# Kernel tuning notes

Hardware: AMD Instinct MI355X
Metric: run time of the kernel (lower is better)

## Reference

```python
import jax, jax.numpy as jnp
import numpy as np

N, C, H, W, HD = 32, 24, 12, 12, 128
GT, FP, A = 256, 256, 28
DIN = (C + 2) * 2 + HD  # 180, g_theta input dim


def setup_inputs() -> dict:
    key = jax.random.key(0)
    ks = jax.random.split(key, 18)
    def w(k, shape):
        fan_in = shape[0]
        return jax.random.normal(k, shape, jnp.float32) / np.sqrt(fan_in).astype(np.float32)
    inp = {
        "x": jax.random.normal(ks[0], (N, C, H, W), jnp.float32),
        "q": jax.random.normal(ks[1], (N, HD), jnp.float32),
        "gW0": w(ks[2], (DIN, GT)), "gb0": jnp.zeros((GT,), jnp.float32),
        "gW1": w(ks[3], (GT, GT)),  "gb1": jnp.zeros((GT,), jnp.float32),
        "gW2": w(ks[4], (GT, GT)),  "gb2": jnp.zeros((GT,), jnp.float32),
        "gW3": w(ks[5], (GT, GT)),  "gb3": jnp.zeros((GT,), jnp.float32),
        "fW0": w(ks[6], (GT, FP)),  "fb0": jnp.zeros((FP,), jnp.float32),
        "fW1": w(ks[7], (FP, FP)),  "fb1": jnp.zeros((FP,), jnp.float32),
        "fW2": w(ks[8], (FP, A)),   "fb2": jnp.zeros((A,), jnp.float32),
    }
    return inp


def _rn_forward(x, q, gW0, gb0, gW1, gb1, gW2, gb2, gW3, gb3,
                fW0, fb0, fW1, fb1, fW2, fb2):
    n, c, h, w = x.shape
    o = h * w
    # rn_encode: per-object features + (x, y) coordinates in [-1, 1]
    feats = x.reshape(n, c, o).transpose(0, 2, 1)            # [n, o, c]
    xc = jnp.repeat(jnp.linspace(-1.0, 1.0, h), w)           # row coord per pixel
    yc = jnp.tile(jnp.linspace(-1.0, 1.0, w), h)             # col coord per pixel
    coords = jnp.stack([xc, yc], axis=-1).astype(x.dtype)    # [o, 2]
    feats = jnp.concatenate([feats, jnp.broadcast_to(coords, (n, o, 2))], axis=-1)  # [n, o, c+2]
    cp = c + 2
    # pairs[n, a, b] = [feats[b], feats[a], q]  (matches torch unsqueeze(1)/unsqueeze(2))
    pairs = jnp.concatenate([
        jnp.broadcast_to(feats[:, None, :, :], (n, o, o, cp)),
        jnp.broadcast_to(feats[:, :, None, :], (n, o, o, cp)),
        jnp.broadcast_to(q[:, None, None, :], (n, o, o, q.shape[1])),
    ], axis=-1)                                              # [n, o, o, 2*cp+hd]
    # g_theta: 4-layer ReLU MLP applied per pair
    hdd = pairs
    for Wm, b in ((gW0, gb0), (gW1, gb1), (gW2, gb2), (gW3, gb3)):
        hdd = jax.nn.relu(jnp.einsum('nabd,de->nabe', hdd, Wm) + b)
    # lower_sum: keep lower-triangular (incl. diagonal) pairs, sum over them
    mask = jnp.tril(jnp.ones((o, o), hdd.dtype))[None, :, :, None]
    rel = jnp.sum(hdd * mask, axis=(1, 2))                   # [n, GT]
    # f_phi: ReLU hidden layers, linear output (dropout = eval mode no-op)
    y = jax.nn.relu(rel @ fW0 + fb0)
    y = jax.nn.relu(y @ fW1 + fb1)
    logits = y @ fW2 + fb2                                   # [n, A]
    return logits


def reference(x, q, gW0, gb0, gW1, gb1, gW2, gb2, gW3, gb3,
              fW0, fb0, fW1, fb1, fW2, fb2):
    return _rn_forward(x, q, gW0, gb0, gW1, gb1, gW2, gb2, gW3, gb3,
                       fW0, fb0, fW1, fb1, fW2, fb2)
```

## Files before the change

kernel.cpp:

```cpp
#include <hip/hip_runtime.h>
#include <hip/hip_bf16.h>

typedef __attribute__((ext_vector_type(8))) short short8;
typedef __attribute__((ext_vector_type(4))) float f32x4;

#define O 144
#define NB 32
#define GT 256
#define NPAIRS 10440
#define TP 128
#define NT 82
#define GRID (NB*NT)
#define CHUNK 328

#define WS_WT   0u
#define WS_U    393216u
#define WS_V    2752512u
#define WS_REL  5144576u
#define WS_CNT  5177344u

__device__ __forceinline__ unsigned short f2bf(float f){
  unsigned int uu = __builtin_bit_cast(unsigned int, f);
  unsigned int lsb = (uu >> 16) & 1u;
  uu += 0x7fffu + lsb;
  return (unsigned short)(uu >> 16);
}
__device__ __forceinline__ unsigned int cvtpk(float lo, float hi){
  unsigned int r;
  asm("v_cvt_pk_bf16_f32 %0, %1, %2" : "=v"(r) : "v"(lo), "v"(hi));
  return r;
}

__global__ void prep_all(const float* __restrict__ x, const float* __restrict__ q,
                         const float* __restrict__ gW0, const float* __restrict__ gb0,
                         const float* __restrict__ gW1, const float* __restrict__ gW2,
                         const float* __restrict__ gW3,
                         unsigned short* __restrict__ u, unsigned short* __restrict__ v,
                         unsigned short* __restrict__ WtP, float* __restrict__ rel,
                         int* __restrict__ cnt){
  int blk = blockIdx.x, t = threadIdx.x;
  if (blk < 256){
    __shared__ float xs[24][18];
    __shared__ float qs[128];
    int n = blk >> 3, oq = blk & 7;
    int o0 = oq * 18;
    for (int i = t; i < 432; i += 256){
      int c = i / 18, oo = i - c*18;
      xs[c][oo] = x[(n*24 + c)*144 + o0 + oo];
    }
    if (t < 128) qs[t] = q[n*128 + t];
    __syncthreads();
    float wq = gb0[t];
    for (int d = 0; d < 128; d++) wq += qs[d] * gW0[(52 + d)*GT + t];
    float wc[52];
    #pragma unroll
    for (int c = 0; c < 52; c++) wc[c] = gW0[c*GT + t];
    for (int oo = 0; oo < 18; oo++){
      int o = o0 + oo;
      float xc = -1.f + 2.f * (float)(o / 12) / 11.f;
      float yc = -1.f + 2.f * (float)(o % 12) / 11.f;
      float su = wq + xc*wc[24] + yc*wc[25];
      float sv =      xc*wc[50] + yc*wc[51];
      #pragma unroll
      for (int c = 0; c < 24; c++){ float f = xs[c][oo]; su += f*wc[c]; sv += f*wc[26+c]; }
      u[(size_t)(n*O + o)*GT + t] = f2bf(su);
      v[(size_t)(n*O + o)*GT + t] = f2bf(sv);
    }
  } else {
    int b2 = blk - 256;
    int li = b2 >> 8, e = b2 & 255;
    int k = t;
    const float* W = (li == 0) ? gW1 : (li == 1) ? gW2 : gW3;
    int et = e >> 4, r = e & 15;
    int kk = k >> 5, g = (k >> 3) & 3, d = k & 7;
    WtP[li*65536 + et*4096 + kk*512 + r*32 + g*8 + d] = f2bf(W[k*GT + e]);
    if (b2 < NB) rel[b2*GT + t] = 0.f;
    if (b2 == 0 && t < NB) cnt[t] = 0;
  }
}

__global__ __launch_bounds__(256, 2) void rn_main(
    const unsigned short* __restrict__ u, const unsigned short* __restrict__ v,
    const unsigned short* __restrict__ WtP,
    const float* __restrict__ gb1, const float* __restrict__ gb2,
    const float* __restrict__ gb3, float* __restrict__ rel, int* __restrict__ cnt,
    const float* __restrict__ fW0, const float* __restrict__ fb0,
    const float* __restrict__ fW1, const float* __restrict__ fb1,
    const float* __restrict__ fW2, const float* __restrict__ fb2,
    float* __restrict__ out)
{
  __shared__ short8 hbuf[4096];
  char* lds = (char*)hbuf;

  const int tid  = threadIdx.x;
  const int lane = tid & 63;
  const int wav  = tid >> 6;
  int lg = (blockIdx.x & 7)*CHUNK + (blockIdx.x >> 3);
  const int n    = lg / NT;
  const int tile = lg - n*NT;
  const int tbase = tile * TP;
  const int l15 = lane & 15, l4 = lane >> 4;

  const unsigned short* wb = WtP + wav*16384 + l15*32 + l4*8;
  short8 aP0,aP1,aP2,aP3, aQ0,aQ1,aQ2,aQ3;
#define LA(s0,s1,s2,s3,p_) { const unsigned short* _wp = wb + ((p_) >> 3)*65536 + ((p_) & 7)*512; \
    s0 = *(const short8*)(_wp);        s1 = *(const short8*)(_wp + 4096); \
    s2 = *(const short8*)(_wp + 8192); s3 = *(const short8*)(_wp + 12288); }
  LA(aP0,aP1,aP2,aP3, 0)
  LA(aQ0,aQ1,aQ2,aQ3, 1)

  {
    int row = wav*32 + (lane >> 1);
    int pt  = tbase + row;
    bool valid = pt < NPAIRS;
    int pa = 0, pb = 0;
    if (valid){
      pa = (int)((sqrtf(8.f*(float)pt + 1.f) - 1.f) * 0.5f);
      while ((pa + 1)*(pa + 2)/2 <= pt) pa++;
      while (pa*(pa + 1)/2 > pt) pa--;
      pb = pt - pa*(pa + 1)/2;
    }
    const uint4* up4 = (const uint4*)(u + (size_t)(n*O + pb)*GT);
    const uint4* vp4 = (const uint4*)(v + (size_t)(n*O + pa)*GT);
    int half = lane & 1;
    int sbase = row*512 + half*256;
    int ts = ((lane >> 1) & 7) << 4;
    #pragma unroll
    for (int cc = 0; cc < 16; cc++){
      uint4 hv;
      if (valid){
        uint4 uu = up4[half*16 + cc];
        uint4 vv = vp4[half*16 + cc];
        #pragma unroll
        for (int j = 0; j < 4; j++){
          unsigned int ud = (&uu.x)[j], vd = (&vv.x)[j];
          float lo = __builtin_bit_cast(float, ud << 16) + __builtin_bit_cast(float, vd << 16);
          float hi = __builtin_bit_cast(float, ud & 0xffff0000u) + __builtin_bit_cast(float, vd & 0xffff0000u);
          (&hv.x)[j] = cvtpk(fmaxf(lo, 0.f), fmaxf(hi, 0.f));
        }
      } else {
        hv = (uint4){0u, 0u, 0u, 0u};
      }
      *(uint4*)(lds + sbase + ((cc*16) ^ ts)) = hv;
    }
  }
  __syncthreads();

  const bool fullvalid = (tbase + TP <= NPAIRS);
  const int swz01 = (l15 & 3) << 4;
  const int swz2  = (l15 & 4) << 4;
  const int rbE = l15*512 + ((l4*16) ^ swz01) + swz2;
  const int rbO = l15*512 + ((l4*16) ^ swz01) - swz2;
  const int ebase = l15*512 + wav*128 + ((l4*8) ^ ((l15 & 1) << 4)) + ((l15 & 6) << 4);
  f32x4 acc[4][8];
  short8 b0[8], b1[8];

#define LOADB(dst_, kk_) { const int rb_ = ((kk_) & 1) ? rbO : rbE; \
    _Pragma("unroll") \
    for (int jp = 0; jp < 8; jp++) dst_[jp] = *(short8*)(lds + rb_ + jp*8192 + (kk_)*64); }

#define MFMAB(bb_, s0,s1,s2,s3) { \
    __builtin_amdgcn_s_setprio(1); \
    _Pragma("unroll") \
    for (int jp = 0; jp < 8; jp++){ \
      acc[0][jp] = __builtin_amdgcn_mfma_f32_16x16x32_bf16(s0, bb_[jp], acc[0][jp], 0, 0, 0); \
      acc[1][jp] = __builtin_amdgcn_mfma_f32_16x16x32_bf16(s1, bb_[jp], acc[1][jp], 0, 0, 0); \
      acc[2][jp] = __builtin_amdgcn_mfma_f32_16x16x32_bf16(s2, bb_[jp], acc[2][jp], 0, 0, 0); \
      acc[3][jp] = __builtin_amdgcn_mfma_f32_16x16x32_bf16(s3, bb_[jp], acc[3][jp], 0, 0, 0); } \
    __builtin_amdgcn_s_setprio(0); }

  #pragma unroll
  for (int L = 0; L < 3; L++){
    const float* gb = (L == 0) ? gb1 : (L == 1) ? gb2 : gb3;

    #pragma unroll
    for (int ie = 0; ie < 4; ie++){
      f32x4 bbv = *(const f32x4*)(gb + wav*64 + ie*16 + l4*4);
      #pragma unroll
      for (int jp = 0; jp < 8; jp++) acc[ie][jp] = bbv;
    }

    LOADB(b0, 0);
    #pragma unroll
    for (int kk = 0; kk < 8; kk++){
      const int p  = L*8 + kk;
      const int pn = (p + 2 > 23) ? 23 : p + 2;
      short8 c0,c1,c2,c3;
      if (p & 1){ c0=aQ0; c1=aQ1; c2=aQ2; c3=aQ3; }
      else      { c0=aP0; c1=aP1; c2=aP2; c3=aP3; }
      if (kk < 7){ if (kk & 1) { LOADB(b0, kk + 1) } else { LOADB(b1, kk + 1) } }
      if (p & 1){ LA(aQ0,aQ1,aQ2,aQ3, pn) } else { LA(aP0,aP1,aP2,aP3, pn) }
      if (kk & 1){ MFMAB(b1, c0,c1,c2,c3) } else { MFMAB(b0, c0,c1,c2,c3) }
    }

    if (L < 2){
      __syncthreads();
      #pragma unroll
      for (int ie = 0; ie < 4; ie++){
        int ea = ebase ^ (ie*32);
        #pragma unroll
        for (int jp = 0; jp < 8; jp++){
          uint2 pk;
          pk.x = cvtpk(fmaxf(acc[ie][jp][0], 0.f), fmaxf(acc[ie][jp][1], 0.f));
          pk.y = cvtpk(fmaxf(acc[ie][jp][2], 0.f), fmaxf(acc[ie][jp][3], 0.f));
          *(uint2*)(lds + ea + jp*8192) = pk;
        }
      }
      __syncthreads();
    } else {
      #pragma unroll
      for (int ie = 0; ie < 4; ie++){
        int e0 = wav*64 + ie*16 + l4*4;
        f32x4 s = {0.f, 0.f, 0.f, 0.f};
        #pragma unroll
        for (int jp = 0; jp < 8; jp++){
          bool pv = fullvalid || (tbase + jp*16 + l15 < NPAIRS);
          #pragma unroll
          for (int j = 0; j < 4; j++){
            float hvv = fmaxf(acc[ie][jp][j], 0.f);
            s[j] += pv ? hvv : 0.f;
          }
        }
        #pragma unroll
        for (int st = 1; st < 16; st <<= 1){
          #pragma unroll
          for (int j = 0; j < 4; j++)
            s[j] += __shfl_xor(s[j], st);
        }
        if (l15 == 0){
          #pragma unroll
          for (int j = 0; j < 4; j++)
            atomicAdd(&rel[n*GT + e0 + j], s[j]);
        }
      }
    }
  }
#undef LA
#undef LOADB
#undef MFMAB

  __syncthreads();
  if (tid == 0) ((int*)lds)[0] = atomicAdd(&cnt[n], 1);
  __syncthreads();
  int done = ((int*)lds)[0];
  __syncthreads();
  if (done == NT - 1){
    float rv = atomicAdd(&rel[n*GT + tid], 0.f);
    float* hsm = (float*)lds;
    float* ysm = hsm + 256;
    int t = tid;
    hsm[t] = rv;
    __syncthreads();
    float s = fb0[t];
    for (int k = 0; k < 256; k++) s += hsm[k] * fW0[k*GT + t];
    ysm[t] = fmaxf(s, 0.f);
    __syncthreads();
    s = fb1[t];
    for (int k = 0; k < 256; k++) s += ysm[k] * fW1[k*GT + t];
    __syncthreads();
    hsm[t] = fmaxf(s, 0.f);
    __syncthreads();
    if (t < 28){
      s = fb2[t];
      for (int k = 0; k < 256; k++) s += hsm[k] * fW2[k*28 + t];
      out[n*28 + t] = s;
    }
  }
}

extern "C" void kernel_launch(void* const* d_in, const int* in_sizes, int n_in,
                              void* d_out, int out_size, void* d_ws, size_t ws_size,
                              hipStream_t stream){
  (void)in_sizes; (void)n_in; (void)out_size; (void)ws_size;
  const float* x   = (const float*)d_in[0];
  const float* q   = (const float*)d_in[1];
  const float* gW0 = (const float*)d_in[2];
  const float* gb0 = (const float*)d_in[3];
  const float* gW1 = (const float*)d_in[4];
  const float* gb1 = (const float*)d_in[5];
  const float* gW2 = (const float*)d_in[6];
  const float* gb2 = (const float*)d_in[7];
  const float* gW3 = (const float*)d_in[8];
  const float* gb3 = (const float*)d_in[9];
  const float* fW0 = (const float*)d_in[10];
  const float* fb0 = (const float*)d_in[11];
  const float* fW1 = (const float*)d_in[12];
  const float* fb1 = (const float*)d_in[13];
  const float* fW2 = (const float*)d_in[14];
  const float* fb2 = (const float*)d_in[15];

  char* ws = (char*)d_ws;
  unsigned short* WtP = (unsigned short*)(ws + WS_WT);
  unsigned short* u   = (unsigned short*)(ws + WS_U);
  unsigned short* v   = (unsigned short*)(ws + WS_V);
  float* rel = (float*)(ws + WS_REL);
  int*   cnt = (int*)(ws + WS_CNT);
  float* out = (float*)d_out;

  hipLaunchKernelGGL(prep_all, dim3(1024), dim3(256), 0, stream,
                     x, q, gW0, gb0, gW1, gW2, gW3, u, v, WtP, rel, cnt);
  hipLaunchKernelGGL(rn_main, dim3(GRID), dim3(256), 0, stream,
                     u, v, WtP, gb1, gb2, gb3, rel, cnt,
                     fW0, fb0, fW1, fb1, fW2, fb2, out);
}
```

Baseline: 260.5 us.

## Split B-fragment loads into halves and shrink A prefetch to one stage

The main MFMA loop now loads the LDS B operand in two halves of four fragments, interleaving each half-load with the MFMAs on the other half, and prefetches the weight A fragments only one K-step ahead instead of two. This lowers register pressure (fewer live short8 buffers) to ease spilling or scheduling at two waves per SIMD, at the cost of less latency hiding for global weight loads. Separately, the prep kernel now computes u/v with one block per batch (32 blocks) instead of 256 blocks, which loads the whole image into LDS but leaves much less parallelism for that phase.

```diff
diff --git a/kernel.cpp b/kernel.cpp
--- a/kernel.cpp
+++ b/kernel.cpp
@@ -39,15 +39,11 @@
                          unsigned short* __restrict__ WtP, float* __restrict__ rel,
                          int* __restrict__ cnt){
   int blk = blockIdx.x, t = threadIdx.x;
-  if (blk < 256){
-    __shared__ float xs[24][18];
+  if (blk < NB){
+    __shared__ float xs[24*144];
     __shared__ float qs[128];
-    int n = blk >> 3, oq = blk & 7;
-    int o0 = oq * 18;
-    for (int i = t; i < 432; i += 256){
-      int c = i / 18, oo = i - c*18;
-      xs[c][oo] = x[(n*24 + c)*144 + o0 + oo];
-    }
+    int n = blk;
+    for (int i = t; i < 24*144; i += 256) xs[i] = x[n*24*144 + i];
     if (t < 128) qs[t] = q[n*128 + t];
     __syncthreads();
     float wq = gb0[t];
@@ -55,19 +51,18 @@
     float wc[52];
     #pragma unroll
     for (int c = 0; c < 52; c++) wc[c] = gW0[c*GT + t];
-    for (int oo = 0; oo < 18; oo++){
-      int o = o0 + oo;
+    for (int o = 0; o < O; o++){
       float xc = -1.f + 2.f * (float)(o / 12) / 11.f;
       float yc = -1.f + 2.f * (float)(o % 12) / 11.f;
       float su = wq + xc*wc[24] + yc*wc[25];
       float sv =      xc*wc[50] + yc*wc[51];
       #pragma unroll
-      for (int c = 0; c < 24; c++){ float f = xs[c][oo]; su += f*wc[c]; sv += f*wc[26+c]; }
+      for (int c = 0; c < 24; c++){ float f = xs[c*144 + o]; su += f*wc[c]; sv += f*wc[26+c]; }
       u[(size_t)(n*O + o)*GT + t] = f2bf(su);
       v[(size_t)(n*O + o)*GT + t] = f2bf(sv);
     }
   } else {
-    int b2 = blk - 256;
+    int b2 = blk - NB;
     int li = b2 >> 8, e = b2 & 255;
     int k = t;
     const float* W = (li == 0) ? gW1 : (li == 1) ? gW2 : gW3;
@@ -102,12 +97,11 @@
   const int l15 = lane & 15, l4 = lane >> 4;
 
   const unsigned short* wb = WtP + wav*16384 + l15*32 + l4*8;
-  short8 aP0,aP1,aP2,aP3, aQ0,aQ1,aQ2,aQ3;
-#define LA(s0,s1,s2,s3,p_) { const unsigned short* _wp = wb + ((p_) >> 3)*65536 + ((p_) & 7)*512; \
-    s0 = *(const short8*)(_wp);        s1 = *(const short8*)(_wp + 4096); \
-    s2 = *(const short8*)(_wp + 8192); s3 = *(const short8*)(_wp + 12288); }
-  LA(aP0,aP1,aP2,aP3, 0)
-  LA(aQ0,aQ1,aQ2,aQ3, 1)
+  short8 an0, an1, an2, an3;
+#define LOADA(p_) { const unsigned short* _wp = wb + ((p_) >> 3)*65536 + ((p_) & 7)*512; \
+    an0 = *(const short8*)(_wp);        an1 = *(const short8*)(_wp + 4096); \
+    an2 = *(const short8*)(_wp + 8192); an3 = *(const short8*)(_wp + 12288); }
+  LOADA(0);
 
   {
     int row = wav*32 + (lane >> 1);
@@ -153,20 +147,20 @@
   const int rbO = l15*512 + ((l4*16) ^ swz01) - swz2;
   const int ebase = l15*512 + wav*128 + ((l4*8) ^ ((l15 & 1) << 4)) + ((l15 & 6) << 4);
   f32x4 acc[4][8];
-  short8 b0[8], b1[8];
-
-#define LOADB(dst_, kk_) { const int rb_ = ((kk_) & 1) ? rbO : rbE; \
+  short8 bA[4], bB[4];
+
+#define LOADBH(dst_, kk_, h_) { const int rb_ = ((kk_) & 1) ? rbO : rbE; \
     _Pragma("unroll") \
-    for (int jp = 0; jp < 8; jp++) dst_[jp] = *(short8*)(lds + rb_ + jp*8192 + (kk_)*64); }
-
-#define MFMAB(bb_, s0,s1,s2,s3) { \
+    for (int jp = 0; jp < 4; jp++) dst_[jp] = *(short8*)(lds + rb_ + (jp + 4*(h_))*8192 + (kk_)*64); }
+
+#define MFMAH(bb_, h_, s0,s1,s2,s3) { \
     __builtin_amdgcn_s_setprio(1); \
     _Pragma("unroll") \
-    for (int jp = 0; jp < 8; jp++){ \
-      acc[0][jp] = __builtin_amdgcn_mfma_f32_16x16x32_bf16(s0, bb_[jp], acc[0][jp], 0, 0, 0); \
-      acc[1][jp] = __builtin_amdgcn_mfma_f32_16x16x32_bf16(s1, bb_[jp], acc[1][jp], 0, 0, 0); \
-      acc[2][jp] = __builtin_amdgcn_mfma_f32_16x16x32_bf16(s2, bb_[jp], acc[2][jp], 0, 0, 0); \
-      acc[3][jp] = __builtin_amdgcn_mfma_f32_16x16x32_bf16(s3, bb_[jp], acc[3][jp], 0, 0, 0); } \
+    for (int jp = 0; jp < 4; jp++){ \
+      acc[0][4*(h_)+jp] = __builtin_amdgcn_mfma_f32_16x16x32_bf16(s0, bb_[jp], acc[0][4*(h_)+jp], 0, 0, 0); \
+      acc[1][4*(h_)+jp] = __builtin_amdgcn_mfma_f32_16x16x32_bf16(s1, bb_[jp], acc[1][4*(h_)+jp], 0, 0, 0); \
+      acc[2][4*(h_)+jp] = __builtin_amdgcn_mfma_f32_16x16x32_bf16(s2, bb_[jp], acc[2][4*(h_)+jp], 0, 0, 0); \
+      acc[3][4*(h_)+jp] = __builtin_amdgcn_mfma_f32_16x16x32_bf16(s3, bb_[jp], acc[3][4*(h_)+jp], 0, 0, 0); } \
     __builtin_amdgcn_s_setprio(0); }
 
   #pragma unroll
@@ -180,17 +174,17 @@
       for (int jp = 0; jp < 8; jp++) acc[ie][jp] = bbv;
     }
 
-    LOADB(b0, 0);
+    LOADBH(bA, 0, 0);
     #pragma unroll
     for (int kk = 0; kk < 8; kk++){
       const int p  = L*8 + kk;
-      const int pn = (p + 2 > 23) ? 23 : p + 2;
-      short8 c0,c1,c2,c3;
-      if (p & 1){ c0=aQ0; c1=aQ1; c2=aQ2; c3=aQ3; }
-      else      { c0=aP0; c1=aP1; c2=aP2; c3=aP3; }
-      if (kk < 7){ if (kk & 1) { LOADB(b0, kk + 1) } else { LOADB(b1, kk + 1) } }
-      if (p & 1){ LA(aQ0,aQ1,aQ2,aQ3, pn) } else { LA(aP0,aP1,aP2,aP3, pn) }
-      if (kk & 1){ MFMAB(b1, c0,c1,c2,c3) } else { MFMAB(b0, c0,c1,c2,c3) }
+      const int pn = (p + 1 > 23) ? 23 : p + 1;
+      short8 a0 = an0, a1 = an1, a2 = an2, a3 = an3;
+      LOADA(pn);
+      LOADBH(bB, kk, 1);
+      MFMAH(bA, 0, a0,a1,a2,a3);
+      if (kk < 7) LOADBH(bA, kk + 1, 0);
+      MFMAH(bB, 1, a0,a1,a2,a3);
     }
 
     if (L < 2){
@@ -235,9 +229,9 @@
       }
     }
   }
-#undef LA
-#undef LOADB
-#undef MFMAB
+#undef LOADA
+#undef LOADBH
+#undef MFMAH
 
   __syncthreads();
   if (tid == 0) ((int*)lds)[0] = atomicAdd(&cnt[n], 1);
@@ -297,7 +291,7 @@
   int*   cnt = (int*)(ws + WS_CNT);
   float* out = (float*)d_out;
 
-  hipLaunchKernelGGL(prep_all, dim3(1024), dim3(256), 0, stream,
+  hipLaunchKernelGGL(prep_all, dim3(800), dim3(256), 0, stream,
                      x, q, gW0, gb0, gW1, gW2, gW3, u, v, WtP, rel, cnt);
   hipLaunchKernelGGL(rn_main, dim3(GRID), dim3(256), 0, stream,
                      u, v, WtP, gb1, gb2, gb3, rel, cnt,
```

Result: slower. 283.2 us (+8.7%).
